# Optimization experiments

Measured on AMD Instinct MI355X. Metric: run time of the kernel, lower is better.

## Reference

```python
import jax, jax.numpy as jnp
import numpy as np

IN_SIZE = 64
NUM_FEATURES = 32
NUM_HEADS = 8
EPS = 1e-5


def setup_inputs() -> dict:
    key = jax.random.key(0)
    ks = jax.random.split(key, 12)
    D, F, Hh = IN_SIZE, NUM_FEATURES, NUM_HEADS
    M = Hh * F  # MLP width = num_heads * num_features
    s = 0.05
    return {
        "x": jax.random.normal(ks[0], (2, D, 48, 48), dtype=jnp.float32),
        # stacked per-head projection weights, stored [in, out]
        "Wq": jax.random.normal(ks[1], (Hh, D, F), dtype=jnp.float32) * s,
        "bq": jax.random.normal(ks[2], (Hh, F), dtype=jnp.float32) * s,
        "Wk": jax.random.normal(ks[3], (Hh, D, F), dtype=jnp.float32) * s,
        "bk": jax.random.normal(ks[4], (Hh, F), dtype=jnp.float32) * s,
        "Wv": jax.random.normal(ks[5], (Hh, D, F), dtype=jnp.float32) * s,
        "bv": jax.random.normal(ks[6], (Hh, F), dtype=jnp.float32) * s,
        "W1": jax.random.normal(ks[7], (M, M), dtype=jnp.float32) * s,
        "b1": jax.random.normal(ks[8], (M,), dtype=jnp.float32) * s,
        "W2": jax.random.normal(ks[9], (M, M), dtype=jnp.float32) * s,
        "b2": jax.random.normal(ks[10], (M,), dtype=jnp.float32) * s,
        "gamma": jnp.ones((M,), dtype=jnp.float32),
        "beta": jnp.zeros((M,), dtype=jnp.float32),
    }


def _inorm_lastdim(y):
    # InstanceNorm1d applied to channels-last tensor: normalizes LAST dim,
    # biased variance, eps=1e-5, no affine.
    mu = jnp.mean(y, axis=-1, keepdims=True)
    var = jnp.mean(jnp.square(y - mu), axis=-1, keepdims=True)
    return (y - mu) / jnp.sqrt(var + EPS)


def reference(x, Wq, bq, Wk, bk, Wv, bv, W1, b1, W2, b2, gamma, beta):
    N, D, H, W = x.shape
    F = NUM_FEATURES
    L = H * W
    flat = jnp.transpose(x, (0, 2, 3, 1)).reshape(N, L, D)  # [N, L, D]

    def proj(Wm, bm):  # Wm [Hh, D, F], bm [Hh, F] -> [Hh, N, L, F]
        y = jnp.einsum('nld,hdf->hnlf', flat, Wm) + bm[:, None, None, :]
        return jax.nn.relu(_inorm_lastdim(y))

    Q = proj(Wq, bq)
    K = proj(Wk, bk)
    V = proj(Wv, bv)

    scores = jnp.einsum('hnlf,hnmf->hnlm', Q, K) / jnp.sqrt(jnp.float32(F))
    # original: F.softmax(scaled) on 3D [N,L,L] -> legacy dim=1 (first L axis)
    att = jax.nn.softmax(scores, axis=2)
    A = jnp.einsum('hnlm,hnmf->hnlf', att, V)  # [Hh, N, L, F]

    heads = jnp.transpose(A, (1, 2, 0, 3)).reshape(N, L, NUM_HEADS * F)
    m = jax.nn.relu(heads @ W1 + b1)
    m = jax.nn.relu(m @ W2 + b2)
    o = _inorm_lastdim(m + heads)
    o = gamma * o + beta  # [N, L, Hh*F]
    return jnp.transpose(o, (0, 2, 1)).reshape(N, NUM_HEADS * F, H, W)
```

## Files before the change

kernel.cpp:

```cpp
#include <hip/hip_runtime.h>
#include <hip/hip_bf16.h>
#include <stdint.h>

#define L_TOT 2304
#define D_IN  64
#define NF    32
#define NH    8
#define NB    2
#define MW    256
#define CHS   8
#define NSTRIP (L_TOT/32)
#define RT    32

constexpr float EPSV  = 1e-5f;
constexpr float SCALE2 = 0.2550351f;

typedef __bf16  bf16x8  __attribute__((ext_vector_type(8)));
typedef float   f32x16  __attribute__((ext_vector_type(16)));

union U32x4BF { uint32_t u[4]; bf16x8 v; };

static __device__ __forceinline__ uint32_t pack_bf16(float a, float b) {
    union { __bf16 h[2]; uint32_t u; } r;
    r.h[0] = (__bf16)a;
    r.h[1] = (__bf16)b;
    return r.u;
}

__global__ void k_prep(const float* __restrict__ W1, const float* __restrict__ W2,
                       __hip_bfloat16* __restrict__ W1t, __hip_bfloat16* __restrict__ W2t)
{
    const float* src = blockIdx.z ? W2 : W1;
    __hip_bfloat16* dst = blockIdx.z ? W2t : W1t;
    __shared__ float t[32][33];
    const int bi = blockIdx.x * 32, bj = blockIdx.y * 32;
    #pragma unroll
    for (int k = 0; k < 4; ++k)
        t[threadIdx.y + 8*k][threadIdx.x] = src[(size_t)(bi + threadIdx.y + 8*k) * MW + bj + threadIdx.x];
    __syncthreads();
    #pragma unroll
    for (int k = 0; k < 4; ++k)
        dst[(size_t)(bj + threadIdx.y + 8*k) * MW + bi + threadIdx.x] =
            __float2bfloat16(t[threadIdx.x][threadIdx.y + 8*k]);
}

__global__ __launch_bounds__(256) void k_prep2(
    const float* __restrict__ x,
    const float* __restrict__ Wq, const float* __restrict__ Wk, const float* __restrict__ Wv,
    __hip_bfloat16* __restrict__ xb, __hip_bfloat16* __restrict__ Wqkvt)
{
    const int job = blockIdx.x;
    const int tx = threadIdx.x & 31, ty = threadIdx.x >> 5;
    const float* src;
    size_t sstride;
    __hip_bfloat16* dst;
    if (job < 24) {
        int mtx = job >> 3, h = job & 7;
        const float* Wm = mtx == 0 ? Wq : (mtx == 1 ? Wk : Wv);
        src = Wm + (size_t)h * D_IN * NF;
        sstride = NF;
        dst = Wqkvt + (size_t)job * NF * D_IN;
    } else {
        int i = job - 24;
        int n = i / NSTRIP, lt = i % NSTRIP;
        src = x + (size_t)n * D_IN * L_TOT + lt * 32;
        sstride = L_TOT;
        dst = xb + ((size_t)n * L_TOT + lt * 32) * D_IN;
    }
    __shared__ float t[64][33];
    #pragma unroll
    for (int k = 0; k < 8; ++k)
        t[ty + 8 * k][tx] = src[(size_t)(ty + 8 * k) * sstride + tx];
    __syncthreads();
    #pragma unroll
    for (int k = 0; k < 4; ++k) {
        int col = ty + 8 * k;
        #pragma unroll
        for (int j = 0; j < 2; ++j)
            dst[(size_t)col * D_IN + tx + 32 * j] = __float2bfloat16(t[tx + 32 * j][col]);
    }
}

__global__ __launch_bounds__(256) void k_proj(
    const __hip_bfloat16* __restrict__ xb, const __hip_bfloat16* __restrict__ Wqkvt,
    const float* __restrict__ bq, const float* __restrict__ bk, const float* __restrict__ bv,
    __hip_bfloat16* __restrict__ Qo, __hip_bfloat16* __restrict__ Ko,
    __hip_bfloat16* __restrict__ Vt)
{
    const int ltile = blockIdx.x;
    const int n = blockIdx.y;
    const int h = blockIdx.z * 4 + (threadIdx.x >> 6);
    const int l0 = ltile * 32;
    const int lane = threadIdx.x & 63;
    const int c = lane & 31, hi = lane >> 5;
    const int hn = h * NB + n;

    const bf16x8* xp = reinterpret_cast<const bf16x8*>(
        xb + ((size_t)n * L_TOT + l0 + c) * D_IN);
    bf16x8 xf[4];
    #pragma unroll
    for (int t = 0; t < 4; ++t) xf[t] = xp[2 * t + hi];

    const float* bs[3] = {bq, bk, bv};

    #pragma unroll
    for (int mtx = 0; mtx < 3; ++mtx) {
        const bf16x8* wp = reinterpret_cast<const bf16x8*>(
            Wqkvt + ((size_t)(mtx * NH + h) * NF + c) * D_IN);
        f32x16 acc = {};
        #pragma unroll
        for (int t = 0; t < 4; ++t)
            acc = __builtin_amdgcn_mfma_f32_32x32x16_bf16(wp[2 * t + hi], xf[t], acc, 0, 0, 0);

        float bb[16];
        #pragma unroll
        for (int g = 0; g < 4; ++g) {
            float4 t4 = *reinterpret_cast<const float4*>(&bs[mtx][h * NF + 8 * g + 4 * hi]);
            bb[4 * g + 0] = t4.x; bb[4 * g + 1] = t4.y;
            bb[4 * g + 2] = t4.z; bb[4 * g + 3] = t4.w;
        }

        float v[16], s = 0.f, s2 = 0.f;
        #pragma unroll
        for (int r = 0; r < 16; ++r) {
            v[r] = acc[r] + bb[r];
            s += v[r]; s2 += v[r] * v[r];
        }
        s  += __shfl_xor(s, 32, 64);
        s2 += __shfl_xor(s2, 32, 64);
        float mu = s * (1.f / 32);
        float rstd = rsqrtf(s2 * (1.f / 32) - mu * mu + EPSV);
        float y[16];
        #pragma unroll
        for (int r = 0; r < 16; ++r) y[r] = fmaxf((v[r] - mu) * rstd, 0.f);

        if (mtx == 2) {
            #pragma unroll
            for (int r = 0; r < 16; ++r) {
                int f = (r & 3) + 8 * (r >> 2) + 4 * hi;
                Vt[((size_t)(hn * NSTRIP + ltile) * NF + f) * 32 + c] = __float2bfloat16(y[r]);
            }
        } else {
            if (mtx == 0) {
                #pragma unroll
                for (int r = 0; r < 16; ++r) y[r] *= SCALE2;
            }
            uint32_t pk[8];
            #pragma unroll
            for (int q = 0; q < 8; ++q) pk[q] = pack_bf16(y[2 * q], y[2 * q + 1]);
            uint32_t rr[4];
            #pragma unroll
            for (int j = 0; j < 4; ++j)
                rr[j] = (uint32_t)__shfl_xor((int)(hi ? pk[j] : pk[4 + j]), 32, 64);
            uint32_t row[8];
            if (hi == 0) {
                row[0] = pk[0]; row[1] = pk[1]; row[2] = rr[0]; row[3] = rr[1];
                row[4] = pk[2]; row[5] = pk[3]; row[6] = rr[2]; row[7] = rr[3];
            } else {
                row[0] = rr[0]; row[1] = rr[1]; row[2] = pk[4]; row[3] = pk[5];
                row[4] = rr[2]; row[5] = rr[3]; row[6] = pk[6]; row[7] = pk[7];
            }
            __hip_bfloat16* dst = (mtx == 0 ? Qo : Ko)
                + ((size_t)hn * L_TOT + l0 + c) * NF + hi * 16;
            reinterpret_cast<uint4*>(dst)[0] = make_uint4(row[0], row[1], row[2], row[3]);
            reinterpret_cast<uint4*>(dst)[1] = make_uint4(row[4], row[5], row[6], row[7]);
        }
    }
}

__global__ __launch_bounds__(256) void k_stats(
    const __hip_bfloat16* __restrict__ Qb, const __hip_bfloat16* __restrict__ Kb,
    float* __restrict__ zpart)
{
    const int w = threadIdx.x >> 6;
    const int strip = blockIdx.x * 4 + w;
    const int hn = blockIdx.y;
    const int chunk = blockIdx.z;
    const int lane = threadIdx.x & 63;
    const int c = lane & 31, hi = lane >> 5;

    const bf16x8* kp = reinterpret_cast<const bf16x8*>(
        Kb + ((size_t)hn * L_TOT + strip * 32 + c) * NF);
    const bf16x8 ka0 = kp[hi];
    const bf16x8 ka1 = kp[2 + hi];

    float Zr[16];
    #pragma unroll
    for (int r = 0; r < 16; ++r) Zr[r] = 0.f;

    for (int it = 0; it < (L_TOT / 32) / CHS; ++it) {
        const int l0 = (chunk * ((L_TOT / 32) / CHS) + it) * 32;
        const bf16x8* qp = reinterpret_cast<const bf16x8*>(
            Qb + ((size_t)hn * L_TOT + l0 + c) * NF);
        bf16x8 qb0 = qp[hi];
        bf16x8 qb1 = qp[2 + hi];
        f32x16 s16 = {};
        s16 = __builtin_amdgcn_mfma_f32_32x32x16_bf16(ka0, qb0, s16, 0, 0, 0);
        s16 = __builtin_amdgcn_mfma_f32_32x32x16_bf16(ka1, qb1, s16, 0, 0, 0);
        #pragma unroll
        for (int r = 0; r < 16; ++r) Zr[r] += exp2f(s16[r]);
    }
    #pragma unroll
    for (int r = 0; r < 16; ++r) {
        #pragma unroll
        for (int o = 16; o >= 1; o >>= 1) Zr[r] += __shfl_xor(Zr[r], o, 64);
    }
    if (c == 0) {
        float4* zp = reinterpret_cast<float4*>(
            zpart + ((size_t)chunk * 16 + hn) * L_TOT + strip * 32 + hi * 16);
        zp[0] = make_float4(Zr[0], Zr[1], Zr[2], Zr[3]);
        zp[1] = make_float4(Zr[4], Zr[5], Zr[6], Zr[7]);
        zp[2] = make_float4(Zr[8], Zr[9], Zr[10], Zr[11]);
        zp[3] = make_float4(Zr[12], Zr[13], Zr[14], Zr[15]);
    }
}

__global__ __launch_bounds__(256) void k_finish(
    const float* __restrict__ zpart, float* __restrict__ zinv)
{
    const int idx = blockIdx.x * 256 + threadIdx.x;
    float Z = 0.f;
    #pragma unroll
    for (int cc = 0; cc < CHS; ++cc) Z += zpart[(size_t)cc * 16 * L_TOT + idx];
    const int p = idx & 31;
    const int hi = (p >> 4) & 1, r = p & 15;
    const int m_local = (r & 3) + 8 * (r >> 2) + 4 * hi;
    zinv[(idx & ~31) + m_local] = 1.f / Z;
}

__global__ __launch_bounds__(256) void k_vscale(
    __hip_bfloat16* __restrict__ Vt, const float* __restrict__ zinv)
{
    const int strip = blockIdx.x, hn = blockIdx.y;
    const int f = threadIdx.x >> 3, mg = (threadIdx.x & 7) * 4;
    const float4 zl = *reinterpret_cast<const float4*>(
        zinv + (size_t)hn * L_TOT + strip * 32 + mg);
    __hip_bfloat16* p = Vt + ((size_t)(hn * NSTRIP + strip) * NF + f) * 32 + mg;
    uint2* p2 = reinterpret_cast<uint2*>(p);
    uint2 old = *p2;
    union { uint2 u2; __bf16 h[4]; } in, outv;
    in.u2 = old;
    outv.h[0] = (__bf16)((float)in.h[0] * zl.x);
    outv.h[1] = (__bf16)((float)in.h[1] * zl.y);
    outv.h[2] = (__bf16)((float)in.h[2] * zl.z);
    outv.h[3] = (__bf16)((float)in.h[3] * zl.w);
    *p2 = outv.u2;
}

__global__ __launch_bounds__(512) void k_apply(
    const __hip_bfloat16* __restrict__ Qb, const __hip_bfloat16* __restrict__ Kb,
    const __hip_bfloat16* __restrict__ Vt,
    float* __restrict__ partA)
{
    const int w = threadIdx.x >> 6;
    const int ltile = blockIdx.x;
    const int l0 = ltile * 32;
    const int hn = blockIdx.y;
    const int lane = threadIdx.x & 63;
    const int c = lane & 31, hi = lane >> 5;

    const bf16x8* qp = reinterpret_cast<const bf16x8*>(
        Qb + ((size_t)hn * L_TOT + l0 + c) * NF);
    const bf16x8 qb0 = qp[hi];
    const bf16x8 qb1 = qp[2 + hi];

    f32x16 acc = {};

    #pragma unroll 3
    for (int it = 0; it < NSTRIP / 8; ++it) {
        const int st = w * (NSTRIP / 8) + it;
        const bf16x8* kp = reinterpret_cast<const bf16x8*>(
            Kb + ((size_t)hn * L_TOT + st * 32 + c) * NF);
        f32x16 s16 = {};
        s16 = __builtin_amdgcn_mfma_f32_32x32x16_bf16(kp[hi], qb0, s16, 0, 0, 0);
        s16 = __builtin_amdgcn_mfma_f32_32x32x16_bf16(kp[2 + hi], qb1, s16, 0, 0, 0);

        float p[16];
        #pragma unroll
        for (int r = 0; r < 16; ++r) p[r] = exp2f(s16[r]);

        uint32_t wp[8];
        #pragma unroll
        for (int q = 0; q < 8; ++q) wp[q] = pack_bf16(p[2 * q], p[2 * q + 1]);

        uint32_t sendA = hi ? wp[0] : wp[2];
        uint32_t sendB = hi ? wp[1] : wp[3];
        uint32_t rA = (uint32_t)__shfl_xor((int)sendA, 32, 64);
        uint32_t rB = (uint32_t)__shfl_xor((int)sendB, 32, 64);
        U32x4BF fragP0;
        fragP0.u[0] = hi ? rA    : wp[0];
        fragP0.u[1] = hi ? rB    : wp[1];
        fragP0.u[2] = hi ? wp[2] : rA;
        fragP0.u[3] = hi ? wp[3] : rB;
        uint32_t sendC = hi ? wp[4] : wp[6];
        uint32_t sendD = hi ? wp[5] : wp[7];
        uint32_t rC = (uint32_t)__shfl_xor((int)sendC, 32, 64);
        uint32_t rD = (uint32_t)__shfl_xor((int)sendD, 32, 64);
        U32x4BF fragP1;
        fragP1.u[0] = hi ? rC    : wp[4];
        fragP1.u[1] = hi ? rD    : wp[5];
        fragP1.u[2] = hi ? wp[6] : rC;
        fragP1.u[3] = hi ? wp[7] : rD;

        const bf16x8* vp = reinterpret_cast<const bf16x8*>(
            Vt + ((size_t)(hn * NSTRIP + st) * NF + c) * 32);
        acc = __builtin_amdgcn_mfma_f32_32x32x16_bf16(fragP0.v, vp[hi], acc, 0, 0, 0);
        acc = __builtin_amdgcn_mfma_f32_32x32x16_bf16(fragP1.v, vp[2 + hi], acc, 0, 0, 0);
    }

    __shared__ float red[8][16][64];
    #pragma unroll
    for (int r = 0; r < 16; ++r) red[w][r][lane] = acc[r];
    __syncthreads();

    const int n = hn & 1, h = hn >> 1;
    float* outp = partA + ((size_t)(n * L_TOT + l0)) * MW + h * NF + c;
    #pragma unroll
    for (int j = 0; j < 2; ++j) {
        const int r = 2 * w + j;
        float sv = 0.f;
        #pragma unroll
        for (int k = 0; k < 8; ++k) sv += red[k][r][lane];
        const int row = (r & 3) + 8 * (r >> 2) + 4 * hi;
        outp[(size_t)row * MW] = sv;
    }
}

__global__ __launch_bounds__(512) void k_mlp(
    const float* __restrict__ partA,
    const __hip_bfloat16* __restrict__ W1t, const float* __restrict__ b1,
    const __hip_bfloat16* __restrict__ W2t, const float* __restrict__ b2,
    const float* __restrict__ gamma, const float* __restrict__ beta,
    float* __restrict__ out)
{
    const int blk = blockIdx.x;
    const int n  = blk / (L_TOT / RT);
    const int l0 = (blk % (L_TOT / RT)) * RT;
    const int tid = threadIdx.x;
    const int w = tid >> 6, lane = tid & 63;
    const int c = lane & 31, hi = lane >> 5;
    const int n0 = w * 32;

    __shared__ __align__(16) char smem[67584];
    float (*hsf)[MW] = reinterpret_cast<float (*)[MW]>(smem);
    __hip_bfloat16 (*hA)[264]  = reinterpret_cast<__hip_bfloat16 (*)[264]>(smem + 32768);
    __hip_bfloat16 (*msb)[264] = reinterpret_cast<__hip_bfloat16 (*)[264]>(smem + 49664);
    float (*ys)[MW] = reinterpret_cast<float (*)[MW]>(smem + 32768);
    float (*rs)[4]  = reinterpret_cast<float (*)[4]>(smem + 66560);
    float (*rs2)[4] = reinterpret_cast<float (*)[4]>(smem + 67072);

    for (int idx = tid; idx < RT * MW; idx += 512) {
        int r = idx >> 8, i = idx & 255;
        float v = partA[((size_t)n * L_TOT + l0 + r) * MW + i];
        hsf[r][i] = v;
        hA[r][i] = __float2bfloat16(v);
    }
    __syncthreads();

    const float bb1 = b1[n0 + c];
    bf16x8 B1[16];
    #pragma unroll
    for (int k0 = 0; k0 < 16; ++k0)
        B1[k0] = *reinterpret_cast<const bf16x8*>(W1t + (size_t)(n0 + c) * MW + k0 * 16 + hi * 8);
    f32x16 acc = {};
    #pragma unroll
    for (int k0 = 0; k0 < 16; ++k0) {
        bf16x8 a = *reinterpret_cast<const bf16x8*>(&hA[c][k0 * 16 + hi * 8]);
        acc = __builtin_amdgcn_mfma_f32_32x32x16_bf16(a, B1[k0], acc, 0, 0, 0);
    }
    #pragma unroll
    for (int r = 0; r < 16; ++r) {
        int row = (r & 3) + 8 * (r >> 2) + 4 * hi;
        msb[row][n0 + c] = __float2bfloat16(fmaxf(acc[r] + bb1, 0.f));
    }
    __syncthreads();

    const float bb2 = b2[n0 + c];
    bf16x8 B2[16];
    #pragma unroll
    for (int k0 = 0; k0 < 16; ++k0)
        B2[k0] = *reinterpret_cast<const bf16x8*>(W2t + (size_t)(n0 + c) * MW + k0 * 16 + hi * 8);
    f32x16 acc2 = {};
    #pragma unroll
    for (int k0 = 0; k0 < 16; ++k0) {
        bf16x8 a = *reinterpret_cast<const bf16x8*>(&msb[c][k0 * 16 + hi * 8]);
        acc2 = __builtin_amdgcn_mfma_f32_32x32x16_bf16(a, B2[k0], acc2, 0, 0, 0);
    }
    float yv[16];
    #pragma unroll
    for (int r = 0; r < 16; ++r) {
        int row = (r & 3) + 8 * (r >> 2) + 4 * hi;
        yv[r] = fmaxf(acc2[r] + bb2, 0.f) + hsf[row][n0 + c];
    }
    __syncthreads();
    #pragma unroll
    for (int r = 0; r < 16; ++r) {
        int row = (r & 3) + 8 * (r >> 2) + 4 * hi;
        ys[row][n0 + c] = yv[r];
    }
    __syncthreads();

    const int col = tid & 255;
    const int half = tid >> 8;
    const int wid = (tid >> 6) & 3;
    float vv[16];
    #pragma unroll
    for (int r = 0; r < 16; ++r) {
        float v = ys[half * 16 + r][col];
        vv[r] = v;
        float s = v, s2 = v * v;
        #pragma unroll
        for (int o = 32; o >= 1; o >>= 1) { s += __shfl_xor(s, o, 64); s2 += __shfl_xor(s2, o, 64); }
        if (lane == 0) { rs[half * 16 + r][wid] = s; rs2[half * 16 + r][wid] = s2; }
    }
    __syncthreads();
    const float g = gamma[col], be = beta[col];
    float ov[16];
    #pragma unroll
    for (int r = 0; r < 16; ++r) {
        int row = half * 16 + r;
        float s  = rs[row][0]  + rs[row][1]  + rs[row][2]  + rs[row][3];
        float s2 = rs2[row][0] + rs2[row][1] + rs2[row][2] + rs2[row][3];
        float mu  = s  * (1.f / MW);
        float var = s2 * (1.f / MW) - mu * mu;
        ov[r] = g * ((vv[r] - mu) * rsqrtf(var + EPSV)) + be;
    }
    float* ob = out + ((size_t)n * MW + col) * L_TOT + l0 + half * 16;
    #pragma unroll
    for (int q = 0; q < 4; ++q)
        reinterpret_cast<float4*>(ob)[q] =
            make_float4(ov[4 * q], ov[4 * q + 1], ov[4 * q + 2], ov[4 * q + 3]);
}

extern "C" void kernel_launch(void* const* d_in, const int* in_sizes, int n_in,
                              void* d_out, int out_size, void* d_ws, size_t ws_size,
                              hipStream_t stream) {
    const float* x  = (const float*)d_in[0];
    const float* Wq = (const float*)d_in[1];
    const float* bq = (const float*)d_in[2];
    const float* Wk = (const float*)d_in[3];
    const float* bk = (const float*)d_in[4];
    const float* Wv = (const float*)d_in[5];
    const float* bv = (const float*)d_in[6];
    const float* W1 = (const float*)d_in[7];
    const float* b1 = (const float*)d_in[8];
    const float* W2 = (const float*)d_in[9];
    const float* b2 = (const float*)d_in[10];
    const float* gm = (const float*)d_in[11];
    const float* bt = (const float*)d_in[12];
    float* out = (float*)d_out;

    const size_t QKVE = (size_t)16 * L_TOT * NF;
    const size_t XBE  = (size_t)NB * L_TOT * D_IN;
    const size_t WQE  = (size_t)3 * NH * NF * D_IN;
    const size_t WTE  = (size_t)MW * MW;
    const size_t ZN = (size_t)CHS * 16 * L_TOT;
    const size_t LN = (size_t)16 * L_TOT;

    __hip_bfloat16* Qb = (__hip_bfloat16*)d_ws;
    __hip_bfloat16* Kb = Qb + QKVE;
    __hip_bfloat16* Vt = Kb + QKVE;
    __hip_bfloat16* xb = Vt + QKVE;
    __hip_bfloat16* Wqkvt = xb + XBE;
    __hip_bfloat16* W1t = Wqkvt + WQE;
    __hip_bfloat16* W2t = W1t + WTE;
    float* zpart = (float*)(W2t + WTE);
    float* zinv  = zpart + ZN;
    float* partA = zinv + LN;

    k_prep<<<dim3(8, 8, 2), dim3(32, 8), 0, stream>>>(W1, W2, W1t, W2t);
    k_prep2<<<dim3(24 + NB * NSTRIP), dim3(256), 0, stream>>>(x, Wq, Wk, Wv, xb, Wqkvt);
    k_proj<<<dim3(NSTRIP, NB, 2), dim3(256), 0, stream>>>(
        xb, Wqkvt, bq, bk, bv, Qb, Kb, Vt);
    k_stats<<<dim3(NSTRIP / 4, 16, CHS), dim3(256), 0, stream>>>(Qb, Kb, zpart);
    k_finish<<<dim3(16 * L_TOT / 256), dim3(256), 0, stream>>>(zpart, zinv);
    k_vscale<<<dim3(NSTRIP, 16), dim3(256), 0, stream>>>(Vt, zinv);
    k_apply<<<dim3(NSTRIP, 16), dim3(512), 0, stream>>>(Qb, Kb, Vt, partA);
    k_mlp<<<dim3(NB * (L_TOT / RT)), dim3(512), 0, stream>>>(
        partA, W1t, b1, W2t, b2, gm, bt, out);
}
```

Baseline: 122.9 us.

## Merge prep kernels, fuse softmax-normalizer into V scaling, split MFMA accumulators

Result: no change. 121.0 us (-1.5%).

```diff
diff --git a/kernel.cpp b/kernel.cpp
--- a/kernel.cpp
+++ b/kernel.cpp
@@ -27,47 +27,51 @@
     return r.u;
 }
 
-__global__ void k_prep(const float* __restrict__ W1, const float* __restrict__ W2,
-                       __hip_bfloat16* __restrict__ W1t, __hip_bfloat16* __restrict__ W2t)
-{
-    const float* src = blockIdx.z ? W2 : W1;
-    __hip_bfloat16* dst = blockIdx.z ? W2t : W1t;
-    __shared__ float t[32][33];
-    const int bi = blockIdx.x * 32, bj = blockIdx.y * 32;
-    #pragma unroll
-    for (int k = 0; k < 4; ++k)
-        t[threadIdx.y + 8*k][threadIdx.x] = src[(size_t)(bi + threadIdx.y + 8*k) * MW + bj + threadIdx.x];
-    __syncthreads();
-    #pragma unroll
-    for (int k = 0; k < 4; ++k)
-        dst[(size_t)(bj + threadIdx.y + 8*k) * MW + bi + threadIdx.x] =
-            __float2bfloat16(t[threadIdx.x][threadIdx.y + 8*k]);
-}
-
-__global__ __launch_bounds__(256) void k_prep2(
+__global__ __launch_bounds__(256) void k_prep(
     const float* __restrict__ x,
     const float* __restrict__ Wq, const float* __restrict__ Wk, const float* __restrict__ Wv,
-    __hip_bfloat16* __restrict__ xb, __hip_bfloat16* __restrict__ Wqkvt)
+    const float* __restrict__ W1, const float* __restrict__ W2,
+    __hip_bfloat16* __restrict__ xb, __hip_bfloat16* __restrict__ Wqkvt,
+    __hip_bfloat16* __restrict__ W1t, __hip_bfloat16* __restrict__ W2t)
 {
     const int job = blockIdx.x;
     const int tx = threadIdx.x & 31, ty = threadIdx.x >> 5;
+    __shared__ float t[64][33];
+
+    if (job < 128) {
+        const int z = job >> 6;
+        const int tt = job & 63;
+        const int bi = (tt >> 3) * 32, bj = (tt & 7) * 32;
+        const float* src = z ? W2 : W1;
+        __hip_bfloat16* dst = z ? W2t : W1t;
+        #pragma unroll
+        for (int k = 0; k < 4; ++k)
+            t[ty + 8 * k][tx] = src[(size_t)(bi + ty + 8 * k) * MW + bj + tx];
+        __syncthreads();
+        #pragma unroll
+        for (int k = 0; k < 4; ++k)
+            dst[(size_t)(bj + ty + 8 * k) * MW + bi + tx] =
+                __float2bfloat16(t[tx][ty + 8 * k]);
+        return;
+    }
+
     const float* src;
     size_t sstride;
     __hip_bfloat16* dst;
-    if (job < 24) {
-        int mtx = job >> 3, h = job & 7;
+    if (job < 152) {
+        int j = job - 128;
+        int mtx = j >> 3, h = j & 7;
         const float* Wm = mtx == 0 ? Wq : (mtx == 1 ? Wk : Wv);
         src = Wm + (size_t)h * D_IN * NF;
         sstride = NF;
-        dst = Wqkvt + (size_t)job * NF * D_IN;
+        dst = Wqkvt + (size_t)j * NF * D_IN;
     } else {
-        int i = job - 24;
+        int i = job - 152;
         int n = i / NSTRIP, lt = i % NSTRIP;
         src = x + (size_t)n * D_IN * L_TOT + lt * 32;
         sstride = L_TOT;
         dst = xb + ((size_t)n * L_TOT + lt * 32) * D_IN;
     }
-    __shared__ float t[64][33];
     #pragma unroll
     for (int k = 0; k < 8; ++k)
         t[ty + 8 * k][tx] = src[(size_t)(ty + 8 * k) * sstride + tx];
@@ -215,36 +219,81 @@
     }
 }
 
-__global__ __launch_bounds__(256) void k_finish(
-    const float* __restrict__ zpart, float* __restrict__ zinv)
-{
-    const int idx = blockIdx.x * 256 + threadIdx.x;
-    float Z = 0.f;
-    #pragma unroll
-    for (int cc = 0; cc < CHS; ++cc) Z += zpart[(size_t)cc * 16 * L_TOT + idx];
-    const int p = idx & 31;
-    const int hi = (p >> 4) & 1, r = p & 15;
-    const int m_local = (r & 3) + 8 * (r >> 2) + 4 * hi;
-    zinv[(idx & ~31) + m_local] = 1.f / Z;
-}
-
-__global__ __launch_bounds__(256) void k_vscale(
-    __hip_bfloat16* __restrict__ Vt, const float* __restrict__ zinv)
+__global__ __launch_bounds__(256) void k_norm(
+    const float* __restrict__ zpart, __hip_bfloat16* __restrict__ Vt)
 {
     const int strip = blockIdx.x, hn = blockIdx.y;
+    __shared__ float zs[CHS][32];
+    __shared__ float zinv_s[32];
+
+    const int cc = threadIdx.x >> 5, p = threadIdx.x & 31;
+    zs[cc][p] = zpart[((size_t)cc * 16 + hn) * L_TOT + strip * 32 + p];
+    __syncthreads();
+    if (threadIdx.x < 32) {
+        const int p2 = threadIdx.x;
+        float Z = 0.f;
+        #pragma unroll
+        for (int k = 0; k < CHS; ++k) Z += zs[k][p2];
+        const int hi = p2 >> 4, r = p2 & 15;
+        const int m_local = (r & 3) + 8 * (r >> 2) + 4 * hi;
+        zinv_s[m_local] = 1.f / Z;
+    }
+    __syncthreads();
+
     const int f = threadIdx.x >> 3, mg = (threadIdx.x & 7) * 4;
-    const float4 zl = *reinterpret_cast<const float4*>(
-        zinv + (size_t)hn * L_TOT + strip * 32 + mg);
-    __hip_bfloat16* p = Vt + ((size_t)(hn * NSTRIP + strip) * NF + f) * 32 + mg;
-    uint2* p2 = reinterpret_cast<uint2*>(p);
-    uint2 old = *p2;
+    __hip_bfloat16* pv = Vt + ((size_t)(hn * NSTRIP + strip) * NF + f) * 32 + mg;
+    uint2* p2v = reinterpret_cast<uint2*>(pv);
     union { uint2 u2; __bf16 h[4]; } in, outv;
-    in.u2 = old;
-    outv.h[0] = (__bf16)((float)in.h[0] * zl.x);
-    outv.h[1] = (__bf16)((float)in.h[1] * zl.y);
-    outv.h[2] = (__bf16)((float)in.h[2] * zl.z);
-    outv.h[3] = (__bf16)((float)in.h[3] * zl.w);
-    *p2 = outv.u2;
+    in.u2 = *p2v;
+    outv.h[0] = (__bf16)((float)in.h[0] * zinv_s[mg + 0]);
+    outv.h[1] = (__bf16)((float)in.h[1] * zinv_s[mg + 1]);
+    outv.h[2] = (__bf16)((float)in.h[2] * zinv_s[mg + 2]);
+    outv.h[3] = (__bf16)((float)in.h[3] * zinv_s[mg + 3]);
+    *p2v = outv.u2;
+}
+
+static __device__ __forceinline__ void apply_strip(
+    int st, int hn, const bf16x8& qb0, const bf16x8& qb1,
+    const __hip_bfloat16* __restrict__ Kb, const __hip_bfloat16* __restrict__ Vt,
+    int c, int hi, f32x16& acc)
+{
+    const bf16x8* kp = reinterpret_cast<const bf16x8*>(
+        Kb + ((size_t)hn * L_TOT + st * 32 + c) * NF);
+    f32x16 s16 = {};
+    s16 = __builtin_amdgcn_mfma_f32_32x32x16_bf16(kp[hi], qb0, s16, 0, 0, 0);
+    s16 = __builtin_amdgcn_mfma_f32_32x32x16_bf16(kp[2 + hi], qb1, s16, 0, 0, 0);
+
+    float p[16];
+    #pragma unroll
+    for (int r = 0; r < 16; ++r) p[r] = exp2f(s16[r]);
+
+    uint32_t wp[8];
+    #pragma unroll
+    for (int q = 0; q < 8; ++q) wp[q] = pack_bf16(p[2 * q], p[2 * q + 1]);
+
+    uint32_t sendA = hi ? wp[0] : wp[2];
+    uint32_t sendB = hi ? wp[1] : wp[3];
+    uint32_t rA = (uint32_t)__shfl_xor((int)sendA, 32, 64);
+    uint32_t rB = (uint32_t)__shfl_xor((int)sendB, 32, 64);
+    U32x4BF fragP0;
+    fragP0.u[0] = hi ? rA    : wp[0];
+    fragP0.u[1] = hi ? rB    : wp[1];
+    fragP0.u[2] = hi ? wp[2] : rA;
+    fragP0.u[3] = hi ? wp[3] : rB;
+    uint32_t sendC = hi ? wp[4] : wp[6];
+    uint32_t sendD = hi ? wp[5] : wp[7];
+    uint32_t rC = (uint32_t)__shfl_xor((int)sendC, 32, 64);
+    uint32_t rD = (uint32_t)__shfl_xor((int)sendD, 32, 64);
+    U32x4BF fragP1;
+    fragP1.u[0] = hi ? rC    : wp[4];
+    fragP1.u[1] = hi ? rD    : wp[5];
+    fragP1.u[2] = hi ? wp[6] : rC;
+    fragP1.u[3] = hi ? wp[7] : rD;
+
+    const bf16x8* vp = reinterpret_cast<const bf16x8*>(
+        Vt + ((size_t)(hn * NSTRIP + st) * NF + c) * 32);
+    acc = __builtin_amdgcn_mfma_f32_32x32x16_bf16(fragP0.v, vp[hi], acc, 0, 0, 0);
+    acc = __builtin_amdgcn_mfma_f32_32x32x16_bf16(fragP1.v, vp[2 + hi], acc, 0, 0, 0);
 }
 
 __global__ __launch_bounds__(512) void k_apply(
@@ -264,53 +313,18 @@
     const bf16x8 qb0 = qp[hi];
     const bf16x8 qb1 = qp[2 + hi];
 
-    f32x16 acc = {};
-
-    #pragma unroll 3
-    for (int it = 0; it < NSTRIP / 8; ++it) {
-        const int st = w * (NSTRIP / 8) + it;
-        const bf16x8* kp = reinterpret_cast<const bf16x8*>(
-            Kb + ((size_t)hn * L_TOT + st * 32 + c) * NF);
-        f32x16 s16 = {};
-        s16 = __builtin_amdgcn_mfma_f32_32x32x16_bf16(kp[hi], qb0, s16, 0, 0, 0);
-        s16 = __builtin_amdgcn_mfma_f32_32x32x16_bf16(kp[2 + hi], qb1, s16, 0, 0, 0);
-
-        float p[16];
-        #pragma unroll
-        for (int r = 0; r < 16; ++r) p[r] = exp2f(s16[r]);
-
-        uint32_t wp[8];
-        #pragma unroll
-        for (int q = 0; q < 8; ++q) wp[q] = pack_bf16(p[2 * q], p[2 * q + 1]);
-
-        uint32_t sendA = hi ? wp[0] : wp[2];
-        uint32_t sendB = hi ? wp[1] : wp[3];
-        uint32_t rA = (uint32_t)__shfl_xor((int)sendA, 32, 64);
-        uint32_t rB = (uint32_t)__shfl_xor((int)sendB, 32, 64);
-        U32x4BF fragP0;
-        fragP0.u[0] = hi ? rA    : wp[0];
-        fragP0.u[1] = hi ? rB    : wp[1];
-        fragP0.u[2] = hi ? wp[2] : rA;
-        fragP0.u[3] = hi ? wp[3] : rB;
-        uint32_t sendC = hi ? wp[4] : wp[6];
-        uint32_t sendD = hi ? wp[5] : wp[7];
-        uint32_t rC = (uint32_t)__shfl_xor((int)sendC, 32, 64);
-        uint32_t rD = (uint32_t)__shfl_xor((int)sendD, 32, 64);
-        U32x4BF fragP1;
-        fragP1.u[0] = hi ? rC    : wp[4];
-        fragP1.u[1] = hi ? rD    : wp[5];
-        fragP1.u[2] = hi ? wp[6] : rC;
-        fragP1.u[3] = hi ? wp[7] : rD;
-
-        const bf16x8* vp = reinterpret_cast<const bf16x8*>(
-            Vt + ((size_t)(hn * NSTRIP + st) * NF + c) * 32);
-        acc = __builtin_amdgcn_mfma_f32_32x32x16_bf16(fragP0.v, vp[hi], acc, 0, 0, 0);
-        acc = __builtin_amdgcn_mfma_f32_32x32x16_bf16(fragP1.v, vp[2 + hi], acc, 0, 0, 0);
-    }
+    f32x16 accA = {}, accB = {};
+    const int sbase = w * (NSTRIP / 8);
+    #pragma unroll
+    for (int it2 = 0; it2 < 4; ++it2) {
+        apply_strip(sbase + 2 * it2,     hn, qb0, qb1, Kb, Vt, c, hi, accA);
+        apply_strip(sbase + 2 * it2 + 1, hn, qb0, qb1, Kb, Vt, c, hi, accB);
+    }
+    apply_strip(sbase + 8, hn, qb0, qb1, Kb, Vt, c, hi, accA);
 
     __shared__ float red[8][16][64];
     #pragma unroll
-    for (int r = 0; r < 16; ++r) red[w][r][lane] = acc[r];
+    for (int r = 0; r < 16; ++r) red[w][r][lane] = accA[r] + accB[r];
     __syncthreads();
 
     const int n = hn & 1, h = hn >> 1;
@@ -362,16 +376,18 @@
     #pragma unroll
     for (int k0 = 0; k0 < 16; ++k0)
         B1[k0] = *reinterpret_cast<const bf16x8*>(W1t + (size_t)(n0 + c) * MW + k0 * 16 + hi * 8);
-    f32x16 acc = {};
-    #pragma unroll
-    for (int k0 = 0; k0 < 16; ++k0) {
-        bf16x8 a = *reinterpret_cast<const bf16x8*>(&hA[c][k0 * 16 + hi * 8]);
-        acc = __builtin_amdgcn_mfma_f32_32x32x16_bf16(a, B1[k0], acc, 0, 0, 0);
+    f32x16 a1 = {}, a1b = {};
+    #pragma unroll
+    for (int k0 = 0; k0 < 8; ++k0) {
+        bf16x8 ae = *reinterpret_cast<const bf16x8*>(&hA[c][(2 * k0) * 16 + hi * 8]);
+        bf16x8 ao = *reinterpret_cast<const bf16x8*>(&hA[c][(2 * k0 + 1) * 16 + hi * 8]);
+        a1  = __builtin_amdgcn_mfma_f32_32x32x16_bf16(ae, B1[2 * k0],     a1,  0, 0, 0);
+        a1b = __builtin_amdgcn_mfma_f32_32x32x16_bf16(ao, B1[2 * k0 + 1], a1b, 0, 0, 0);
     }
     #pragma unroll
     for (int r = 0; r < 16; ++r) {
         int row = (r & 3) + 8 * (r >> 2) + 4 * hi;
-        msb[row][n0 + c] = __float2bfloat16(fmaxf(acc[r] + bb1, 0.f));
+        msb[row][n0 + c] = __float2bfloat16(fmaxf(a1[r] + a1b[r] + bb1, 0.f));
     }
     __syncthreads();
 
@@ -380,17 +396,19 @@
     #pragma unroll
     for (int k0 = 0; k0 < 16; ++k0)
         B2[k0] = *reinterpret_cast<const bf16x8*>(W2t + (size_t)(n0 + c) * MW + k0 * 16 + hi * 8);
-    f32x16 acc2 = {};
-    #pragma unroll
-    for (int k0 = 0; k0 < 16; ++k0) {
-        bf16x8 a = *reinterpret_cast<const bf16x8*>(&msb[c][k0 * 16 + hi * 8]);
-        acc2 = __builtin_amdgcn_mfma_f32_32x32x16_bf16(a, B2[k0], acc2, 0, 0, 0);
+    f32x16 a2 = {}, a2b = {};
+    #pragma unroll
+    for (int k0 = 0; k0 < 8; ++k0) {
+        bf16x8 ae = *reinterpret_cast<const bf16x8*>(&msb[c][(2 * k0) * 16 + hi * 8]);
+        bf16x8 ao = *reinterpret_cast<const bf16x8*>(&msb[c][(2 * k0 + 1) * 16 + hi * 8]);
+        a2  = __builtin_amdgcn_mfma_f32_32x32x16_bf16(ae, B2[2 * k0],     a2,  0, 0, 0);
+        a2b = __builtin_amdgcn_mfma_f32_32x32x16_bf16(ao, B2[2 * k0 + 1], a2b, 0, 0, 0);
     }
     float yv[16];
     #pragma unroll
     for (int r = 0; r < 16; ++r) {
         int row = (r & 3) + 8 * (r >> 2) + 4 * hi;
-        yv[r] = fmaxf(acc2[r] + bb2, 0.f) + hsf[row][n0 + c];
+        yv[r] = fmaxf(a2[r] + a2b[r] + bb2, 0.f) + hsf[row][n0 + c];
     }
     __syncthreads();
     #pragma unroll
@@ -455,7 +473,6 @@
     const size_t WQE  = (size_t)3 * NH * NF * D_IN;
     const size_t WTE  = (size_t)MW * MW;
     const size_t ZN = (size_t)CHS * 16 * L_TOT;
-    const size_t LN = (size_t)16 * L_TOT;
 
     __hip_bfloat16* Qb = (__hip_bfloat16*)d_ws;
     __hip_bfloat16* Kb = Qb + QKVE;
@@ -465,16 +482,14 @@
     __hip_bfloat16* W1t = Wqkvt + WQE;
     __hip_bfloat16* W2t = W1t + WTE;
     float* zpart = (float*)(W2t + WTE);
-    float* zinv  = zpart + ZN;
-    float* partA = zinv + LN;
-
-    k_prep<<<dim3(8, 8, 2), dim3(32, 8), 0, stream>>>(W1, W2, W1t, W2t);
-    k_prep2<<<dim3(24 + NB * NSTRIP), dim3(256), 0, stream>>>(x, Wq, Wk, Wv, xb, Wqkvt);
+    float* partA = zpart + ZN;
+
+    k_prep<<<dim3(296), dim3(256), 0, stream>>>(
+        x, Wq, Wk, Wv, W1, W2, xb, Wqkvt, W1t, W2t);
     k_proj<<<dim3(NSTRIP, NB, 2), dim3(256), 0, stream>>>(
         xb, Wqkvt, bq, bk, bv, Qb, Kb, Vt);
     k_stats<<<dim3(NSTRIP / 4, 16, CHS), dim3(256), 0, stream>>>(Qb, Kb, zpart);
-    k_finish<<<dim3(16 * L_TOT / 256), dim3(256), 0, stream>>>(zpart, zinv);
-    k_vscale<<<dim3(NSTRIP, 16), dim3(256), 0, stream>>>(Vt, zinv);
+    k_norm<<<dim3(NSTRIP, 16), dim3(256), 0, stream>>>(zpart, Vt);
     k_apply<<<dim3(NSTRIP, 16), dim3(512), 0, stream>>>(Qb, Kb, Vt, partA);
     k_mlp<<<dim3(NB * (L_TOT / RT)), dim3(512), 0, stream>>>(
         partA, W1t, b1, W2t, b2, gm, bt, out);
```
